# Kernel tuning notes

Measured on AMD Instinct MI355X. Metric: run time of the kernel, lower is better.

The kernel has to match this reference:

```python
import jax, jax.numpy as jnp
import numpy as np

N_NODES = 100000


def gcn_conv(x, W, b, src, dst, n_nodes):
    """PyG GCNConv: add self-loops, symmetric deg^-1/2 normalization,
    linear transform then gather->scale->scatter-add, plus bias."""
    h = x @ W  # [N, out] - transform first (small GEMM), propagate after
    loop = jnp.arange(n_nodes, dtype=src.dtype)
    s = jnp.concatenate([src, loop])  # sources incl. self-loops
    d = jnp.concatenate([dst, loop])  # targets incl. self-loops
    deg = jax.ops.segment_sum(jnp.ones_like(d, dtype=h.dtype), d,
                              num_segments=n_nodes)  # in-degree on augmented graph
    dinv = jnp.where(deg > 0, jax.lax.rsqrt(deg), 0.0)
    norm = dinv[s] * dinv[d]  # [E+N]
    msg = h[s] * norm[:, None]  # gather + per-edge scale
    out = jax.ops.segment_sum(msg, d, num_segments=n_nodes)  # scatter-add
    return out + b


def setup_inputs() -> dict:
    key = jax.random.key(0)
    ks = jax.random.split(key, 8)
    in_dim, hid = 128, 128
    n_edges = 1600000
    x = jax.random.normal(ks[0], (N_NODES, in_dim), dtype=jnp.float32)
    edge_index = jax.random.randint(ks[1], (2, n_edges), 0, N_NODES, dtype=jnp.int64)
    s1 = 1.0 / np.sqrt(in_dim)
    s2 = 1.0 / np.sqrt(hid)
    W1 = jax.random.uniform(ks[2], (in_dim, hid), jnp.float32, -s1, s1)
    b1 = jnp.zeros((hid,), jnp.float32)
    W2 = jax.random.uniform(ks[3], (hid, 2), jnp.float32, -s2, s2)
    b2 = jnp.zeros((2,), jnp.float32)
    W_skip = jax.random.uniform(ks[4], (in_dim, 2), jnp.float32, -s1, s1)
    b_skip = jnp.zeros((2,), jnp.float32)
    return {"x": x, "edge_index": edge_index, "W1": W1, "b1": b1,
            "W2": W2, "b2": b2, "W_skip": W_skip, "b_skip": b_skip}


def reference(x, edge_index, W1, b1, W2, b2, W_skip, b_skip):
    src, dst = edge_index[0], edge_index[1]
    h = gcn_conv(x, W1, b1, src, dst, N_NODES)
    h = jax.nn.relu(h)
    # dropout is identity in eval mode (training=False)
    out = gcn_conv(h, W2, b2, src, dst, N_NODES)
    out = out + x @ W_skip + b_skip
    return out
```

## Files before the change

kernel.cpp:

```cpp
#include <hip/hip_runtime.h>

#define NN 100000
#define NB 196
#define BSHIFT 9
#define BMASK 511

typedef __attribute__((ext_vector_type(8))) short short8;
typedef __attribute__((ext_vector_type(4))) float f32x4;

__device__ __forceinline__ unsigned short f2bf(float f) {
  union { float f; unsigned int u; } v;
  v.f = f;
  unsigned int r = (v.u + 0x7fffu + ((v.u >> 16) & 1u)) >> 16;
  return (unsigned short)r;
}
__device__ __forceinline__ float bf_lo(unsigned int u) {
  union { unsigned int u; float f; } v;
  v.u = u << 16;
  return v.f;
}
__device__ __forceinline__ float bf_hi(unsigned int u) {
  union { unsigned int u; float f; } v;
  v.u = u & 0xffff0000u;
  return v.f;
}

__global__ __launch_bounds__(512) void k_bucket(const float* __restrict__ W1,
                                                unsigned short* __restrict__ pw,
                                                const int* __restrict__ src,
                                                const int* __restrict__ dst, int E,
                                                int cap, int* __restrict__ bcur,
                                                unsigned int* __restrict__ bkt) {
  if (blockIdx.x < 4) {
    int idx = blockIdx.x * 512 + threadIdx.x;
    int lane = idx & 63, f = idx >> 6;
    int nt = f >> 2, ks = f & 3;
    int n = nt * 16 + (lane & 15);
    int k0 = ks * 32 + (lane >> 4) * 8;
    unsigned short tmp[8];
#pragma unroll
    for (int j = 0; j < 8; ++j) tmp[j] = f2bf(W1[(k0 + j) * 128 + n]);
    *(uint4*)&pw[idx * 8] = *(uint4*)tmp;
    return;
  }
  __shared__ int cnt_l[NB];
  __shared__ int start_l[NB];
  __shared__ int gbase[NB];
  __shared__ int wsum2[8];
  __shared__ unsigned int stage[4096];
  __shared__ int addr[4096];
  const int t = threadIdx.x;
  const int lane = t & 63, wid = t >> 6;
  for (int i = t; i < NB; i += 512) cnt_l[i] = 0;
  __syncthreads();
  const int nblk = gridDim.x - 4;
  const int nbatch = (E + 4095) >> 12;
  for (int bi = blockIdx.x - 4; bi < nbatch; bi += nblk) {
    const int e0 = bi << 12;
    unsigned int ent[8];
    int bb[8], pp[8];
#pragma unroll
    for (int j = 0; j < 8; ++j) {
      int e = e0 + j * 512 + t;
      if (e < E) {
        int d = dst[e], s = src[e];
        bb[j] = d >> BSHIFT;
        ent[j] = ((unsigned int)s << BSHIFT) | (unsigned int)(d & BMASK);
        pp[j] = atomicAdd(&cnt_l[bb[j]], 1);
      } else {
        bb[j] = -1;
      }
    }
    __syncthreads();
    int v = (t < NB) ? cnt_l[t] : 0;
    if (t < NB) gbase[t] = atomicAdd(&bcur[t], v);
    int incl = v;
#pragma unroll
    for (int off = 1; off < 64; off <<= 1) {
      int u = __shfl_up(incl, off);
      if (lane >= off) incl += u;
    }
    if (lane == 63) wsum2[wid] = incl;
    __syncthreads();
    int wpre = 0;
#pragma unroll
    for (int j = 0; j < 8; ++j) wpre += (j < wid) ? wsum2[j] : 0;
    int tot = wsum2[0] + wsum2[1] + wsum2[2] + wsum2[3] +
              wsum2[4] + wsum2[5] + wsum2[6] + wsum2[7];
    if (t < NB) start_l[t] = wpre + incl - v;
    __syncthreads();
#pragma unroll
    for (int j = 0; j < 8; ++j) {
      if (bb[j] >= 0) {
        int slot = start_l[bb[j]] + pp[j];
        stage[slot] = ent[j];
        addr[slot] = bb[j] * cap + gbase[bb[j]] + pp[j];
      }
    }
    __syncthreads();
    for (int s2 = t; s2 < tot; s2 += 512) bkt[addr[s2]] = stage[s2];
    __syncthreads();
    for (int i = t; i < NB; i += 512) cnt_l[i] = 0;
    __syncthreads();
  }
}

__global__ __launch_bounds__(512) void k_scatter(const int* __restrict__ bcur,
                                                 const unsigned int* __restrict__ bkt,
                                                 int cap, int* __restrict__ total,
                                                 int* __restrict__ ofs,
                                                 int* __restrict__ cnt,
                                                 float* __restrict__ dinv,
                                                 int* __restrict__ bin, int n) {
  __shared__ int hist[512];
  __shared__ int sofs[512];
  __shared__ int wsum[8];
  __shared__ int base;
  const int b = blockIdx.x;
  const int t = threadIdx.x;
  const int lane = t & 63, wid = t >> 6;
  hist[t] = 0;
  __syncthreads();
  const int m = bcur[b];
  const unsigned int* p = &bkt[(size_t)b * cap];
  for (int i = t; i < m; i += 512) atomicAdd(&hist[p[i] & BMASK], 1);
  __syncthreads();
  int c = hist[t];
  int cp = (c + 7) & ~7;
  int incl = cp;
#pragma unroll
  for (int off = 1; off < 64; off <<= 1) {
    int u = __shfl_up(incl, off);
    if (lane >= off) incl += u;
  }
  if (lane == 63) wsum[wid] = incl;
  __syncthreads();
  if (t == 0) {
    int run = 0;
#pragma unroll
    for (int j = 0; j < 8; ++j) { int s = wsum[j]; wsum[j] = run; run += s; }
    base = atomicAdd(total, run);
  }
  __syncthreads();
  int exc = base + wsum[wid] + incl - cp;
  sofs[t] = exc;
  int node = (b << BSHIFT) + t;
  if (node < n) {
    ofs[node] = exc;
    cnt[node] = c;
    dinv[node] = rsqrtf((float)c + 1.0f);
  }
  hist[t] = 0;
  __syncthreads();
  for (int p2 = c; p2 < cp; ++p2) bin[exc + p2] = n;
  for (int i = t; i < m; i += 512) {
    unsigned int u = p[i];
    int dl = u & BMASK;
    int pos = atomicAdd(&hist[dl], 1);
    bin[sofs[dl] + pos] = (int)(u >> BSHIFT);
  }
}

__global__ __launch_bounds__(256) void k_gemm1(const float* __restrict__ x,
                                               const uint4* __restrict__ pw4,
                                               const float* __restrict__ W_skip,
                                               const float* __restrict__ dinv,
                                               unsigned short* __restrict__ hA16,
                                               float* __restrict__ skipout, int N) {
  __shared__ __align__(16) unsigned short Bs[16384];
  __shared__ float Ws[256];
  const int t = threadIdx.x;
#pragma unroll
  for (int it = 0; it < 8; ++it) {
    int idx = t + it * 256;
    *(uint4*)&Bs[idx * 8] = pw4[idx];
  }
  Ws[t] = W_skip[t];
  __syncthreads();

  const int lane = t & 63, w = t >> 6;
  const int m = lane & 15, q = lane >> 4;
  const int grow = blockIdx.x * 64 + w * 16 + m;
  const bool valid = grow < N;
  const float* xp = &x[(size_t)(valid ? grow : 0) * 128];

  f32x4 acc[8];
#pragma unroll
  for (int nt = 0; nt < 8; ++nt) acc[nt] = (f32x4){0.f, 0.f, 0.f, 0.f};
  float sk0 = 0.f, sk1 = 0.f;

#pragma unroll
  for (int ks = 0; ks < 4; ++ks) {
    short8 a;
    const int kb = ks * 32 + q * 8;
    if (valid) {
      const float* p = xp + kb;
      float4 f0 = *(const float4*)p;
      float4 f1 = *(const float4*)(p + 4);
      a[0] = (short)f2bf(f0.x); a[1] = (short)f2bf(f0.y);
      a[2] = (short)f2bf(f0.z); a[3] = (short)f2bf(f0.w);
      a[4] = (short)f2bf(f1.x); a[5] = (short)f2bf(f1.y);
      a[6] = (short)f2bf(f1.z); a[7] = (short)f2bf(f1.w);
      sk0 += f0.x * Ws[(kb + 0) * 2] + f0.y * Ws[(kb + 1) * 2] +
             f0.z * Ws[(kb + 2) * 2] + f0.w * Ws[(kb + 3) * 2] +
             f1.x * Ws[(kb + 4) * 2] + f1.y * Ws[(kb + 5) * 2] +
             f1.z * Ws[(kb + 6) * 2] + f1.w * Ws[(kb + 7) * 2];
      sk1 += f0.x * Ws[(kb + 0) * 2 + 1] + f0.y * Ws[(kb + 1) * 2 + 1] +
             f0.z * Ws[(kb + 2) * 2 + 1] + f0.w * Ws[(kb + 3) * 2 + 1] +
             f1.x * Ws[(kb + 4) * 2 + 1] + f1.y * Ws[(kb + 5) * 2 + 1] +
             f1.z * Ws[(kb + 6) * 2 + 1] + f1.w * Ws[(kb + 7) * 2 + 1];
    } else {
      a = (short8)0;
    }
#pragma unroll
    for (int nt = 0; nt < 8; ++nt) {
      short8 bfr = *(const short8*)&Bs[((nt * 4 + ks) * 64 + lane) * 8];
      acc[nt] = __builtin_amdgcn_mfma_f32_16x16x32_bf16(a, bfr, acc[nt], 0, 0, 0);
    }
  }

  sk0 += __shfl_xor(sk0, 16); sk0 += __shfl_xor(sk0, 32);
  sk1 += __shfl_xor(sk1, 16); sk1 += __shfl_xor(sk1, 32);
  if (valid && q == 0) *(float2*)&skipout[grow * 2] = make_float2(sk0, sk1);

  const int orow = blockIdx.x * 64 + w * 16 + q * 4;
  float4 dv = *(const float4*)&dinv[orow];
  float dvr[4] = {dv.x, dv.y, dv.z, dv.w};
#pragma unroll
  for (int nt = 0; nt < 8; ++nt) {
    int col = nt * 16 + m;
#pragma unroll
    for (int rg = 0; rg < 4; ++rg) {
      int rr = orow + rg;
      if (rr < N) hA16[(size_t)rr * 128 + col] = f2bf(acc[nt][rg] * dvr[rg]);
    }
  }
}

__global__ __launch_bounds__(256) void k_gather1(const int* __restrict__ ofs,
                                                 const int* __restrict__ cnt,
                                                 const int* __restrict__ bin,
                                                 const float* __restrict__ dinv,
                                                 const uint4* __restrict__ hp,
                                                 const float* __restrict__ b1,
                                                 const float* __restrict__ W2,
                                                 float* __restrict__ t2s, int N) {
  int d = blockIdx.x * 4 + (threadIdx.x >> 6);
  if (d >= N) return;
  const int lane = threadIdx.x & 63;
  const int rg = lane >> 4;
  const int fl = lane & 15;
  const int beg = ofs[d];
  const int np = (cnt[d] + 7) & ~7;

  const float dd = dinv[d];
  uint4 vs = hp[(size_t)d * 16 + fl];
  float4 b1a = *(const float4*)&b1[fl * 8];
  float4 b1b = *(const float4*)&b1[fl * 8 + 4];
  float4 wa = *(const float4*)&W2[fl * 16];
  float4 wb = *(const float4*)&W2[fl * 16 + 4];
  float4 wc = *(const float4*)&W2[fl * 16 + 8];
  float4 wd = *(const float4*)&W2[fl * 16 + 12];

  float acc[8] = {};
  for (int e0 = 0; e0 < np; e0 += 8) {
    int s0 = bin[beg + e0 + rg];
    int s1 = bin[beg + e0 + 4 + rg];
    uint4 v0 = hp[(size_t)s0 * 16 + fl];
    uint4 v1 = hp[(size_t)s1 * 16 + fl];
    acc[0] += bf_lo(v0.x); acc[1] += bf_hi(v0.x);
    acc[2] += bf_lo(v0.y); acc[3] += bf_hi(v0.y);
    acc[4] += bf_lo(v0.z); acc[5] += bf_hi(v0.z);
    acc[6] += bf_lo(v0.w); acc[7] += bf_hi(v0.w);
    acc[0] += bf_lo(v1.x); acc[1] += bf_hi(v1.x);
    acc[2] += bf_lo(v1.y); acc[3] += bf_hi(v1.y);
    acc[4] += bf_lo(v1.z); acc[5] += bf_hi(v1.z);
    acc[6] += bf_lo(v1.w); acc[7] += bf_hi(v1.w);
  }
#pragma unroll
  for (int j = 0; j < 8; ++j) {
    acc[j] += __shfl_xor(acc[j], 16);
    acc[j] += __shfl_xor(acc[j], 32);
  }
  acc[0] += bf_lo(vs.x); acc[1] += bf_hi(vs.x);
  acc[2] += bf_lo(vs.y); acc[3] += bf_hi(vs.y);
  acc[4] += bf_lo(vs.z); acc[5] += bf_hi(vs.z);
  acc[6] += bf_lo(vs.w); acc[7] += bf_hi(vs.w);

  float vj[8];
  vj[0] = fmaxf(acc[0] * dd + b1a.x, 0.f);
  vj[1] = fmaxf(acc[1] * dd + b1a.y, 0.f);
  vj[2] = fmaxf(acc[2] * dd + b1a.z, 0.f);
  vj[3] = fmaxf(acc[3] * dd + b1a.w, 0.f);
  vj[4] = fmaxf(acc[4] * dd + b1b.x, 0.f);
  vj[5] = fmaxf(acc[5] * dd + b1b.y, 0.f);
  vj[6] = fmaxf(acc[6] * dd + b1b.z, 0.f);
  vj[7] = fmaxf(acc[7] * dd + b1b.w, 0.f);
  float p0 = vj[0] * wa.x + vj[1] * wa.z + vj[2] * wb.x + vj[3] * wb.z +
             vj[4] * wc.x + vj[5] * wc.z + vj[6] * wd.x + vj[7] * wd.z;
  float p1 = vj[0] * wa.y + vj[1] * wa.w + vj[2] * wb.y + vj[3] * wb.w +
             vj[4] * wc.y + vj[5] * wc.w + vj[6] * wd.y + vj[7] * wd.w;
#pragma unroll
  for (int off = 1; off < 16; off <<= 1) {
    p0 += __shfl_xor(p0, off);
    p1 += __shfl_xor(p1, off);
  }
  if (lane == 0) *(float2*)&t2s[d * 2] = make_float2(p0 * dd, p1 * dd);
}

__global__ __launch_bounds__(256) void k_final(const float* __restrict__ b_skip,
                                               const float* __restrict__ b2,
                                               const float* __restrict__ t2s,
                                               const float* __restrict__ skipout,
                                               const float* __restrict__ dinv,
                                               const int* __restrict__ ofs,
                                               const int* __restrict__ cnt,
                                               const int* __restrict__ bin,
                                               float* __restrict__ out, int N) {
  int i = blockIdx.x * 4 + (threadIdx.x >> 6);
  if (i >= N) return;
  const int lane = threadIdx.x & 63;
  const int beg = ofs[i], end = beg + cnt[i];
  float g0 = 0.f, g1 = 0.f;
  for (int e = beg + lane; e < end; e += 64) {
    int s = bin[e];
    float2 t = *(const float2*)&t2s[s * 2];
    g0 += t.x; g1 += t.y;
  }
#pragma unroll
  for (int off = 32; off > 0; off >>= 1) {
    g0 += __shfl_down(g0, off);
    g1 += __shfl_down(g1, off);
  }
  if (lane == 0) {
    float di = dinv[i];
    float2 ts = *(const float2*)&t2s[i * 2];
    float2 sk = *(const float2*)&skipout[i * 2];
    float o0 = di * (g0 + ts.x) + b2[0] + sk.x + b_skip[0];
    float o1 = di * (g1 + ts.y) + b2[1] + sk.y + b_skip[1];
    *(float2*)&out[i * 2] = make_float2(o0, o1);
  }
}

extern "C" void kernel_launch(void* const* d_in, const int* in_sizes, int n_in,
                              void* d_out, int out_size, void* d_ws, size_t ws_size,
                              hipStream_t stream) {
  const float* x      = (const float*)d_in[0];
  const int*   edges  = (const int*)d_in[1];
  const float* W1     = (const float*)d_in[2];
  const float* b1     = (const float*)d_in[3];
  const float* W2     = (const float*)d_in[4];
  const float* b2     = (const float*)d_in[5];
  const float* W_skip = (const float*)d_in[6];
  const float* b_skip = (const float*)d_in[7];
  float* out = (float*)d_out;

  const int N = NN;
  const int E = in_sizes[1] / 2;
  const int* src = edges;
  const int* dst = edges + E;
  const size_t BINCAP = (size_t)E + 8 * (size_t)N;
  const int CAP = (((E + NB - 1) / NB) + 1280 + 255) & ~255;

  unsigned short* hA16 = (unsigned short*)d_ws;
  int*   bcur    = (int*)(hA16 + (size_t)(NN + 1) * 128);
  int*   total   = bcur + NB;
  int*   ofs     = total + 4;
  float* dinv    = (float*)(ofs + N + 4);
  int*   cnt     = (int*)(dinv + N);
  unsigned int* bkt = (unsigned int*)(cnt + N);
  int*   bin     = (int*)(bkt + (size_t)NB * CAP);
  float* t2s     = (float*)(bin + BINCAP);
  float* skipout = t2s + 2 * (size_t)N;
  unsigned short* pw = (unsigned short*)(skipout + 2 * (size_t)N);

  hipMemsetAsync(hA16 + (size_t)N * 128, 0, 256 + (NB + 4) * sizeof(int), stream);

  const int nbatch = (E + 4095) / 4096;
  k_bucket<<<4 + nbatch, 512, 0, stream>>>(W1, pw, src, dst, E, CAP, bcur, bkt);
  k_scatter<<<NB, 512, 0, stream>>>(bcur, bkt, CAP, total, ofs, cnt, dinv, bin, N);
  k_gemm1<<<(N + 63) / 64, 256, 0, stream>>>(x, (const uint4*)pw, W_skip, dinv, hA16,
                                             skipout, N);
  k_gather1<<<(N + 3) / 4, 256, 0, stream>>>(ofs, cnt, bin, dinv, (const uint4*)hA16,
                                             b1, W2, t2s, N);
  k_final<<<(N + 3) / 4, 256, 0, stream>>>(b_skip, b2, t2s, skipout, dinv, ofs, cnt,
                                           bin, out, N);
}
```

Measured before the change: 245.4 us.

## Merge edge bucketing and layer-1 GEMM into one launch, move dinv scaling to gather

Edge bucketing and the first-layer GEMM now run in a single launch, with blocks split by index and shared memory overlaid through a union, so the GEMM no longer waits for degree computation. Because the GEMM runs before degrees are known, it drops the source-side dinv scaling. The gather instead loads dinv[src] per edge and applies it with FMAs, with a dinv[n]=0 sentinel for padding entries. The bucket count doubles to 391 with 256 nodes each and the per-bucket capacity is changed, and every GEMM block reconverts W1 to bf16 itself. This adds one extra scalar load per edge in the gather in exchange for one fewer launch and overlapped work.

```diff
diff --git a/kernel.cpp b/kernel.cpp
--- a/kernel.cpp
+++ b/kernel.cpp
@@ -1,9 +1,9 @@
 #include <hip/hip_runtime.h>
 
 #define NN 100000
-#define NB 196
-#define BSHIFT 9
-#define BMASK 511
+#define NB 391
+#define BSHIFT 8
+#define BMASK 255
 
 typedef __attribute__((ext_vector_type(8))) short short8;
 typedef __attribute__((ext_vector_type(4))) float f32x4;
@@ -25,37 +25,39 @@
   return v.f;
 }
 
-__global__ __launch_bounds__(512) void k_bucket(const float* __restrict__ W1,
-                                                unsigned short* __restrict__ pw,
-                                                const int* __restrict__ src,
+union SMem {
+  struct {
+    int cnt_l[NB];
+    int start_l[NB];
+    int gbase[NB];
+    int wsum2[8];
+    unsigned int stage[4096];
+    int addr[4096];
+  } b;
+  struct {
+    unsigned short Bs[16384];
+    float Ws[256];
+  } g;
+};
+
+__global__ __launch_bounds__(512) void k_phase1(const int* __restrict__ src,
                                                 const int* __restrict__ dst, int E,
                                                 int cap, int* __restrict__ bcur,
-                                                unsigned int* __restrict__ bkt) {
-  if (blockIdx.x < 4) {
-    int idx = blockIdx.x * 512 + threadIdx.x;
-    int lane = idx & 63, f = idx >> 6;
-    int nt = f >> 2, ks = f & 3;
-    int n = nt * 16 + (lane & 15);
-    int k0 = ks * 32 + (lane >> 4) * 8;
-    unsigned short tmp[8];
-#pragma unroll
-    for (int j = 0; j < 8; ++j) tmp[j] = f2bf(W1[(k0 + j) * 128 + n]);
-    *(uint4*)&pw[idx * 8] = *(uint4*)tmp;
-    return;
-  }
-  __shared__ int cnt_l[NB];
-  __shared__ int start_l[NB];
-  __shared__ int gbase[NB];
-  __shared__ int wsum2[8];
-  __shared__ unsigned int stage[4096];
-  __shared__ int addr[4096];
+                                                unsigned int* __restrict__ bkt,
+                                                const float* __restrict__ x,
+                                                const float* __restrict__ W1,
+                                                const float* __restrict__ W_skip,
+                                                unsigned short* __restrict__ hA16,
+                                                float* __restrict__ skipout, int N,
+                                                int nbatch) {
+  __shared__ __align__(16) SMem sm;
   const int t = threadIdx.x;
   const int lane = t & 63, wid = t >> 6;
-  for (int i = t; i < NB; i += 512) cnt_l[i] = 0;
-  __syncthreads();
-  const int nblk = gridDim.x - 4;
-  const int nbatch = (E + 4095) >> 12;
-  for (int bi = blockIdx.x - 4; bi < nbatch; bi += nblk) {
+
+  if ((int)blockIdx.x < nbatch) {
+    for (int i = t; i < NB; i += 512) sm.b.cnt_l[i] = 0;
+    __syncthreads();
+    const int bi = blockIdx.x;
     const int e0 = bi << 12;
     unsigned int ent[8];
     int bb[8], pp[8];
@@ -66,121 +68,60 @@
         int d = dst[e], s = src[e];
         bb[j] = d >> BSHIFT;
         ent[j] = ((unsigned int)s << BSHIFT) | (unsigned int)(d & BMASK);
-        pp[j] = atomicAdd(&cnt_l[bb[j]], 1);
+        pp[j] = atomicAdd(&sm.b.cnt_l[bb[j]], 1);
       } else {
         bb[j] = -1;
       }
     }
     __syncthreads();
-    int v = (t < NB) ? cnt_l[t] : 0;
-    if (t < NB) gbase[t] = atomicAdd(&bcur[t], v);
+    int v = (t < NB) ? sm.b.cnt_l[t] : 0;
+    if (t < NB) sm.b.gbase[t] = atomicAdd(&bcur[t], v);
     int incl = v;
 #pragma unroll
     for (int off = 1; off < 64; off <<= 1) {
       int u = __shfl_up(incl, off);
       if (lane >= off) incl += u;
     }
-    if (lane == 63) wsum2[wid] = incl;
+    if (lane == 63) sm.b.wsum2[wid] = incl;
     __syncthreads();
     int wpre = 0;
 #pragma unroll
-    for (int j = 0; j < 8; ++j) wpre += (j < wid) ? wsum2[j] : 0;
-    int tot = wsum2[0] + wsum2[1] + wsum2[2] + wsum2[3] +
-              wsum2[4] + wsum2[5] + wsum2[6] + wsum2[7];
-    if (t < NB) start_l[t] = wpre + incl - v;
+    for (int j = 0; j < 8; ++j) wpre += (j < wid) ? sm.b.wsum2[j] : 0;
+    int tot = sm.b.wsum2[0] + sm.b.wsum2[1] + sm.b.wsum2[2] + sm.b.wsum2[3] +
+              sm.b.wsum2[4] + sm.b.wsum2[5] + sm.b.wsum2[6] + sm.b.wsum2[7];
+    if (t < NB) sm.b.start_l[t] = wpre + incl - v;
     __syncthreads();
 #pragma unroll
     for (int j = 0; j < 8; ++j) {
       if (bb[j] >= 0) {
-        int slot = start_l[bb[j]] + pp[j];
-        stage[slot] = ent[j];
-        addr[slot] = bb[j] * cap + gbase[bb[j]] + pp[j];
+        int slot = sm.b.start_l[bb[j]] + pp[j];
+        sm.b.stage[slot] = ent[j];
+        sm.b.addr[slot] = bb[j] * cap + sm.b.gbase[bb[j]] + pp[j];
       }
     }
     __syncthreads();
-    for (int s2 = t; s2 < tot; s2 += 512) bkt[addr[s2]] = stage[s2];
-    __syncthreads();
-    for (int i = t; i < NB; i += 512) cnt_l[i] = 0;
-    __syncthreads();
-  }
-}
-
-__global__ __launch_bounds__(512) void k_scatter(const int* __restrict__ bcur,
-                                                 const unsigned int* __restrict__ bkt,
-                                                 int cap, int* __restrict__ total,
-                                                 int* __restrict__ ofs,
-                                                 int* __restrict__ cnt,
-                                                 float* __restrict__ dinv,
-                                                 int* __restrict__ bin, int n) {
-  __shared__ int hist[512];
-  __shared__ int sofs[512];
-  __shared__ int wsum[8];
-  __shared__ int base;
-  const int b = blockIdx.x;
-  const int t = threadIdx.x;
-  const int lane = t & 63, wid = t >> 6;
-  hist[t] = 0;
-  __syncthreads();
-  const int m = bcur[b];
-  const unsigned int* p = &bkt[(size_t)b * cap];
-  for (int i = t; i < m; i += 512) atomicAdd(&hist[p[i] & BMASK], 1);
-  __syncthreads();
-  int c = hist[t];
-  int cp = (c + 7) & ~7;
-  int incl = cp;
-#pragma unroll
-  for (int off = 1; off < 64; off <<= 1) {
-    int u = __shfl_up(incl, off);
-    if (lane >= off) incl += u;
-  }
-  if (lane == 63) wsum[wid] = incl;
-  __syncthreads();
-  if (t == 0) {
-    int run = 0;
-#pragma unroll
-    for (int j = 0; j < 8; ++j) { int s = wsum[j]; wsum[j] = run; run += s; }
-    base = atomicAdd(total, run);
-  }
-  __syncthreads();
-  int exc = base + wsum[wid] + incl - cp;
-  sofs[t] = exc;
-  int node = (b << BSHIFT) + t;
-  if (node < n) {
-    ofs[node] = exc;
-    cnt[node] = c;
-    dinv[node] = rsqrtf((float)c + 1.0f);
-  }
-  hist[t] = 0;
-  __syncthreads();
-  for (int p2 = c; p2 < cp; ++p2) bin[exc + p2] = n;
-  for (int i = t; i < m; i += 512) {
-    unsigned int u = p[i];
-    int dl = u & BMASK;
-    int pos = atomicAdd(&hist[dl], 1);
-    bin[sofs[dl] + pos] = (int)(u >> BSHIFT);
-  }
-}
-
-__global__ __launch_bounds__(256) void k_gemm1(const float* __restrict__ x,
-                                               const uint4* __restrict__ pw4,
-                                               const float* __restrict__ W_skip,
-                                               const float* __restrict__ dinv,
-                                               unsigned short* __restrict__ hA16,
-                                               float* __restrict__ skipout, int N) {
-  __shared__ __align__(16) unsigned short Bs[16384];
-  __shared__ float Ws[256];
-  const int t = threadIdx.x;
-#pragma unroll
-  for (int it = 0; it < 8; ++it) {
-    int idx = t + it * 256;
-    *(uint4*)&Bs[idx * 8] = pw4[idx];
-  }
-  Ws[t] = W_skip[t];
-  __syncthreads();
-
-  const int lane = t & 63, w = t >> 6;
+    for (int s2 = t; s2 < tot; s2 += 512) bkt[sm.b.addr[s2]] = sm.b.stage[s2];
+    return;
+  }
+
+  const int rb = blockIdx.x - nbatch;
+#pragma unroll
+  for (int it = 0; it < 4; ++it) {
+    int idx = t + it * 512;
+    int l2 = idx & 63, f = idx >> 6;
+    int nt = f >> 2, ks = f & 3;
+    int nn = nt * 16 + (l2 & 15);
+    int k0 = ks * 32 + (l2 >> 4) * 8;
+    unsigned short tmp[8];
+#pragma unroll
+    for (int j = 0; j < 8; ++j) tmp[j] = f2bf(W1[(k0 + j) * 128 + nn]);
+    *(uint4*)&sm.g.Bs[idx * 8] = *(uint4*)tmp;
+  }
+  if (t < 256) sm.g.Ws[t] = W_skip[t];
+  __syncthreads();
+
   const int m = lane & 15, q = lane >> 4;
-  const int grow = blockIdx.x * 64 + w * 16 + m;
+  const int grow = rb * 128 + wid * 16 + m;
   const bool valid = grow < N;
   const float* xp = &x[(size_t)(valid ? grow : 0) * 128];
 
@@ -201,20 +142,20 @@
       a[2] = (short)f2bf(f0.z); a[3] = (short)f2bf(f0.w);
       a[4] = (short)f2bf(f1.x); a[5] = (short)f2bf(f1.y);
       a[6] = (short)f2bf(f1.z); a[7] = (short)f2bf(f1.w);
-      sk0 += f0.x * Ws[(kb + 0) * 2] + f0.y * Ws[(kb + 1) * 2] +
-             f0.z * Ws[(kb + 2) * 2] + f0.w * Ws[(kb + 3) * 2] +
-             f1.x * Ws[(kb + 4) * 2] + f1.y * Ws[(kb + 5) * 2] +
-             f1.z * Ws[(kb + 6) * 2] + f1.w * Ws[(kb + 7) * 2];
-      sk1 += f0.x * Ws[(kb + 0) * 2 + 1] + f0.y * Ws[(kb + 1) * 2 + 1] +
-             f0.z * Ws[(kb + 2) * 2 + 1] + f0.w * Ws[(kb + 3) * 2 + 1] +
-             f1.x * Ws[(kb + 4) * 2 + 1] + f1.y * Ws[(kb + 5) * 2 + 1] +
-             f1.z * Ws[(kb + 6) * 2 + 1] + f1.w * Ws[(kb + 7) * 2 + 1];
+      sk0 += f0.x * sm.g.Ws[(kb + 0) * 2] + f0.y * sm.g.Ws[(kb + 1) * 2] +
+             f0.z * sm.g.Ws[(kb + 2) * 2] + f0.w * sm.g.Ws[(kb + 3) * 2] +
+             f1.x * sm.g.Ws[(kb + 4) * 2] + f1.y * sm.g.Ws[(kb + 5) * 2] +
+             f1.z * sm.g.Ws[(kb + 6) * 2] + f1.w * sm.g.Ws[(kb + 7) * 2];
+      sk1 += f0.x * sm.g.Ws[(kb + 0) * 2 + 1] + f0.y * sm.g.Ws[(kb + 1) * 2 + 1] +
+             f0.z * sm.g.Ws[(kb + 2) * 2 + 1] + f0.w * sm.g.Ws[(kb + 3) * 2 + 1] +
+             f1.x * sm.g.Ws[(kb + 4) * 2 + 1] + f1.y * sm.g.Ws[(kb + 5) * 2 + 1] +
+             f1.z * sm.g.Ws[(kb + 6) * 2 + 1] + f1.w * sm.g.Ws[(kb + 7) * 2 + 1];
     } else {
       a = (short8)0;
     }
 #pragma unroll
     for (int nt = 0; nt < 8; ++nt) {
-      short8 bfr = *(const short8*)&Bs[((nt * 4 + ks) * 64 + lane) * 8];
+      short8 bfr = *(const short8*)&sm.g.Bs[((nt * 4 + ks) * 64 + lane) * 8];
       acc[nt] = __builtin_amdgcn_mfma_f32_16x16x32_bf16(a, bfr, acc[nt], 0, 0, 0);
     }
   }
@@ -223,17 +164,74 @@
   sk1 += __shfl_xor(sk1, 16); sk1 += __shfl_xor(sk1, 32);
   if (valid && q == 0) *(float2*)&skipout[grow * 2] = make_float2(sk0, sk1);
 
-  const int orow = blockIdx.x * 64 + w * 16 + q * 4;
-  float4 dv = *(const float4*)&dinv[orow];
-  float dvr[4] = {dv.x, dv.y, dv.z, dv.w};
+  const int orow = rb * 128 + wid * 16 + q * 4;
 #pragma unroll
   for (int nt = 0; nt < 8; ++nt) {
     int col = nt * 16 + m;
 #pragma unroll
     for (int rg = 0; rg < 4; ++rg) {
       int rr = orow + rg;
-      if (rr < N) hA16[(size_t)rr * 128 + col] = f2bf(acc[nt][rg] * dvr[rg]);
-    }
+      if (rr < N) hA16[(size_t)rr * 128 + col] = f2bf(acc[nt][rg]);
+    }
+  }
+}
+
+__global__ __launch_bounds__(512) void k_scatter(const int* __restrict__ bcur,
+                                                 const unsigned int* __restrict__ bkt,
+                                                 int cap, int* __restrict__ total,
+                                                 int* __restrict__ ofs,
+                                                 int* __restrict__ cnt,
+                                                 float* __restrict__ dinv,
+                                                 int* __restrict__ bin, int n) {
+  __shared__ int hist[256];
+  __shared__ int sofs[256];
+  __shared__ int wsum[8];
+  __shared__ int base;
+  const int b = blockIdx.x;
+  const int t = threadIdx.x;
+  const int lane = t & 63, wid = t >> 6;
+  if (t < 256) hist[t] = 0;
+  __syncthreads();
+  const int m = bcur[b];
+  const unsigned int* p = &bkt[(size_t)b * cap];
+  for (int i = t; i < m; i += 512) atomicAdd(&hist[p[i] & BMASK], 1);
+  __syncthreads();
+  int c = (t < 256) ? hist[t] : 0;
+  int cp = (c + 7) & ~7;
+  int incl = cp;
+#pragma unroll
+  for (int off = 1; off < 64; off <<= 1) {
+    int u = __shfl_up(incl, off);
+    if (lane >= off) incl += u;
+  }
+  if (lane == 63) wsum[wid] = incl;
+  __syncthreads();
+  if (t == 0) {
+    int run = 0;
+#pragma unroll
+    for (int j = 0; j < 8; ++j) { int s = wsum[j]; wsum[j] = run; run += s; }
+    base = atomicAdd(total, run);
+  }
+  __syncthreads();
+  int exc = base + wsum[wid] + incl - cp;
+  if (t < 256) {
+    sofs[t] = exc;
+    int node = (b << BSHIFT) + t;
+    if (node < n) {
+      ofs[node] = exc;
+      cnt[node] = c;
+      dinv[node] = rsqrtf((float)c + 1.0f);
+    }
+    hist[t] = 0;
+  }
+  if (b == 0 && t == 300) dinv[n] = 0.f;
+  __syncthreads();
+  for (int p2 = c; p2 < cp; ++p2) bin[exc + p2] = n;
+  for (int i = t; i < m; i += 512) {
+    unsigned int u = p[i];
+    int dl = u & BMASK;
+    int pos = atomicAdd(&hist[dl], 1);
+    bin[sofs[dl] + pos] = (int)(u >> BSHIFT);
   }
 }
 
@@ -266,26 +264,28 @@
   for (int e0 = 0; e0 < np; e0 += 8) {
     int s0 = bin[beg + e0 + rg];
     int s1 = bin[beg + e0 + 4 + rg];
+    float w0 = dinv[s0];
+    float w1 = dinv[s1];
     uint4 v0 = hp[(size_t)s0 * 16 + fl];
     uint4 v1 = hp[(size_t)s1 * 16 + fl];
-    acc[0] += bf_lo(v0.x); acc[1] += bf_hi(v0.x);
-    acc[2] += bf_lo(v0.y); acc[3] += bf_hi(v0.y);
-    acc[4] += bf_lo(v0.z); acc[5] += bf_hi(v0.z);
-    acc[6] += bf_lo(v0.w); acc[7] += bf_hi(v0.w);
-    acc[0] += bf_lo(v1.x); acc[1] += bf_hi(v1.x);
-    acc[2] += bf_lo(v1.y); acc[3] += bf_hi(v1.y);
-    acc[4] += bf_lo(v1.z); acc[5] += bf_hi(v1.z);
-    acc[6] += bf_lo(v1.w); acc[7] += bf_hi(v1.w);
+    acc[0] = fmaf(w0, bf_lo(v0.x), acc[0]); acc[1] = fmaf(w0, bf_hi(v0.x), acc[1]);
+    acc[2] = fmaf(w0, bf_lo(v0.y), acc[2]); acc[3] = fmaf(w0, bf_hi(v0.y), acc[3]);
+    acc[4] = fmaf(w0, bf_lo(v0.z), acc[4]); acc[5] = fmaf(w0, bf_hi(v0.z), acc[5]);
+    acc[6] = fmaf(w0, bf_lo(v0.w), acc[6]); acc[7] = fmaf(w0, bf_hi(v0.w), acc[7]);
+    acc[0] = fmaf(w1, bf_lo(v1.x), acc[0]); acc[1] = fmaf(w1, bf_hi(v1.x), acc[1]);
+    acc[2] = fmaf(w1, bf_lo(v1.y), acc[2]); acc[3] = fmaf(w1, bf_hi(v1.y), acc[3]);
+    acc[4] = fmaf(w1, bf_lo(v1.z), acc[4]); acc[5] = fmaf(w1, bf_hi(v1.z), acc[5]);
+    acc[6] = fmaf(w1, bf_lo(v1.w), acc[6]); acc[7] = fmaf(w1, bf_hi(v1.w), acc[7]);
   }
 #pragma unroll
   for (int j = 0; j < 8; ++j) {
     acc[j] += __shfl_xor(acc[j], 16);
     acc[j] += __shfl_xor(acc[j], 32);
   }
-  acc[0] += bf_lo(vs.x); acc[1] += bf_hi(vs.x);
-  acc[2] += bf_lo(vs.y); acc[3] += bf_hi(vs.y);
-  acc[4] += bf_lo(vs.z); acc[5] += bf_hi(vs.z);
-  acc[6] += bf_lo(vs.w); acc[7] += bf_hi(vs.w);
+  acc[0] = fmaf(dd, bf_lo(vs.x), acc[0]); acc[1] = fmaf(dd, bf_hi(vs.x), acc[1]);
+  acc[2] = fmaf(dd, bf_lo(vs.y), acc[2]); acc[3] = fmaf(dd, bf_hi(vs.y), acc[3]);
+  acc[4] = fmaf(dd, bf_lo(vs.z), acc[4]); acc[5] = fmaf(dd, bf_hi(vs.z), acc[5]);
+  acc[6] = fmaf(dd, bf_lo(vs.w), acc[6]); acc[7] = fmaf(dd, bf_hi(vs.w), acc[7]);
 
   float vj[8];
   vj[0] = fmaxf(acc[0] * dd + b1a.x, 0.f);
@@ -360,27 +360,26 @@
   const int* src = edges;
   const int* dst = edges + E;
   const size_t BINCAP = (size_t)E + 8 * (size_t)N;
-  const int CAP = (((E + NB - 1) / NB) + 1280 + 255) & ~255;
+  const int CAP = ((E / NB) + 896 + 255) & ~255;
 
   unsigned short* hA16 = (unsigned short*)d_ws;
   int*   bcur    = (int*)(hA16 + (size_t)(NN + 1) * 128);
   int*   total   = bcur + NB;
   int*   ofs     = total + 4;
   float* dinv    = (float*)(ofs + N + 4);
-  int*   cnt     = (int*)(dinv + N);
+  int*   cnt     = (int*)(dinv + N + 8);
   unsigned int* bkt = (unsigned int*)(cnt + N);
   int*   bin     = (int*)(bkt + (size_t)NB * CAP);
   float* t2s     = (float*)(bin + BINCAP);
   float* skipout = t2s + 2 * (size_t)N;
-  unsigned short* pw = (unsigned short*)(skipout + 2 * (size_t)N);
 
   hipMemsetAsync(hA16 + (size_t)N * 128, 0, 256 + (NB + 4) * sizeof(int), stream);
 
   const int nbatch = (E + 4095) / 4096;
-  k_bucket<<<4 + nbatch, 512, 0, stream>>>(W1, pw, src, dst, E, CAP, bcur, bkt);
+  const int gemmb = (N + 127) / 128;
+  k_phase1<<<nbatch + gemmb, 512, 0, stream>>>(src, dst, E, CAP, bcur, bkt, x, W1,
+                                               W_skip, hA16, skipout, N, nbatch);
   k_scatter<<<NB, 512, 0, stream>>>(bcur, bkt, CAP, total, ofs, cnt, dinv, bin, N);
-  k_gemm1<<<(N + 63) / 64, 256, 0, stream>>>(x, (const uint4*)pw, W_skip, dinv, hA16,
-                                             skipout, N);
   k_gather1<<<(N + 3) / 4, 256, 0, stream>>>(ofs, cnt, bin, dinv, (const uint4*)hA16,
                                              b1, W2, t2s, N);
   k_final<<<(N + 3) / 4, 256, 0, stream>>>(b_skip, b2, t2s, skipout, dinv, ofs, cnt,
```

New measurement: 242.1 us. No clear change (-1.3%).
